# Kernel optimization log

Measured on AMD Instinct MI355X. Metric: run time of the kernel, lower is better.

The kernel has to match this reference:

```python
import jax, jax.numpy as jnp
from jax import lax
import numpy as np

NA, NC = 3, 1
CONF_THRESH, IOU_THRESH = 0.5, 0.5


def _conv(x, w, b, pad):
    y = lax.conv_general_dilated(x, w, (1, 1), [(pad, pad), (pad, pad)],
                                 dimension_numbers=('NCHW', 'OIHW', 'NCHW'))
    return y + b[None, :, None, None]


def _maxpool2(x):
    return lax.reduce_window(x, -jnp.inf, lax.max, (1, 1, 2, 2), (1, 1, 2, 2), 'VALID')


def _stream(x, w1, b1, w2, b2):
    x = _maxpool2(jax.nn.relu(_conv(x, w1, b1, 1)))
    x = _maxpool2(jax.nn.relu(_conv(x, w2, b2, 1)))
    return x


def _pairwise_iou(b):
    # b: [N,4] in (x1,y1,x2,y2); matches torchvision box_iou (no area clamp)
    x1, y1, x2, y2 = b[:, 0], b[:, 1], b[:, 2], b[:, 3]
    area = (x2 - x1) * (y2 - y1)
    ix1 = jnp.maximum(x1[:, None], x1[None, :])
    iy1 = jnp.maximum(y1[:, None], y1[None, :])
    ix2 = jnp.minimum(x2[:, None], x2[None, :])
    iy2 = jnp.minimum(y2[:, None], y2[None, :])
    inter = jnp.clip(ix2 - ix1, 0.0) * jnp.clip(iy2 - iy1, 0.0)
    return inter / (area[:, None] + area[None, :] - inter)


def _nms_keep(boxes, scores, conf_keep, iou_thresh):
    # Greedy NMS over a fixed, small N; returns bool keep mask (conf + NMS).
    n = boxes.shape[0]
    order = jnp.argsort(-jnp.where(conf_keep, scores, -jnp.inf))
    iou = _pairwise_iou(boxes[order])  # [N,N] in score order
    idx = jnp.arange(n)

    def body(i, state):
        keep, suppressed = state
        valid = jnp.logical_not(suppressed[i])
        keep = keep.at[i].set(valid)
        suppressed = suppressed | (valid & (iou[i] > iou_thresh) & (idx > i))
        return keep, suppressed

    keep_sorted, _ = lax.fori_loop(0, n, body,
                                   (jnp.zeros(n, bool), jnp.zeros(n, bool)))
    keep = jnp.zeros(n, bool).at[order].set(keep_sorted)
    return keep & conf_keep


def setup_inputs() -> dict:
    key = jax.random.key(0)
    ks = jax.random.split(key, 14)
    s = 0.05
    inp = {
        'x': jax.random.normal(ks[0], (8, 3, 512, 512), jnp.float32),
        'rgb_w1': jax.random.normal(ks[1], (32, 3, 3, 3), jnp.float32) * s,
        'rgb_b1': jnp.zeros((32,), jnp.float32),
        'rgb_w2': jax.random.normal(ks[2], (64, 32, 3, 3), jnp.float32) * s,
        'rgb_b2': jnp.zeros((64,), jnp.float32),
        'ir_w1': jax.random.normal(ks[3], (32, 3, 3, 3), jnp.float32) * s,
        'ir_b1': jnp.zeros((32,), jnp.float32),
        'ir_w2': jax.random.normal(ks[4], (64, 32, 3, 3), jnp.float32) * s,
        'ir_b2': jnp.zeros((64,), jnp.float32),
        'fuse_w': jax.random.normal(ks[5], (128, 128, 3, 3), jnp.float32) * s,
        'fuse_b': jnp.zeros((128,), jnp.float32),
        'det_w': jax.random.normal(ks[6], (NA * (5 + NC), 128, 1, 1), jnp.float32),
        'det_b': jax.random.normal(ks[7], (NA * (5 + NC),), jnp.float32),
    }
    return inp


def reference(x, rgb_w1, rgb_b1, rgb_w2, rgb_b2,
              ir_w1, ir_b1, ir_w2, ir_b2,
              fuse_w, fuse_b, det_w, det_b):
    f1 = _stream(x, rgb_w1, rgb_b1, rgb_w2, rgb_b2)   # [B,64,H/4,W/4]
    f2 = _stream(x, ir_w1, ir_b1, ir_w2, ir_b2)       # [B,64,H/4,W/4]
    f = jnp.concatenate([f1, f2], axis=1)             # [B,128,H/4,W/4]
    f = jax.nn.relu(_conv(f, fuse_w, fuse_b, 1))
    f = jnp.mean(f, axis=(2, 3), keepdims=True)       # AdaptiveAvgPool2d((1,1))
    p = _conv(f, det_w, det_b, 0)                     # [B,18,1,1]
    B, C, H, W = p.shape
    p = p.reshape(B, NA, 5 + NC, H, W).transpose(0, 1, 3, 4, 2)  # [B,na,H,W,5+nc]
    boxes = p[..., :4].reshape(B, -1, 4)              # [B, na*H*W, 4]
    scores = jax.nn.sigmoid(p[..., 4]).reshape(B, -1) # [B, na*H*W]
    conf_keep = scores > CONF_THRESH
    keep = jax.vmap(_nms_keep, in_axes=(0, 0, 0, None))(boxes, scores, conf_keep,
                                                        IOU_THRESH)
    # Fixed-shape equivalent of the per-image variable-length preds list:
    # preds[b] == boxes[b][keep[b]].
    return p, boxes, scores, keep
```

## Files before the change

kernel.cpp:

```cpp
#include <hip/hip_runtime.h>
#include <math.h>


typedef __bf16 bf16x8 __attribute__((ext_vector_type(8)));
typedef float f32x4 __attribute__((ext_vector_type(4)));

static __device__ __forceinline__ ushort f2bf(float f) {
    unsigned u = __float_as_uint(f);
    unsigned r = (u + 0x7fffu + ((u >> 16) & 1u)) >> 16;
    return (ushort)r;
}
static __device__ __forceinline__ float bf2f(ushort h) {
    return __uint_as_float(((unsigned)h) << 16);
}

__global__ __launch_bounds__(256) void conv1_pool(
    const float* __restrict__ x, const float* __restrict__ w,
    const float* __restrict__ bias, ushort* __restrict__ C1h,
    ushort* __restrict__ C1l)
{
    __shared__ float s[3 * 34 * 34];
    const int b = blockIdx.z;
    const int tileX = blockIdx.x, tileY = blockIdx.y;
    const int tid = threadIdx.x;
    const int tx = tid & 15, ty = tid >> 4;
    const int ih0 = tileY * 32 - 1, iw0 = tileX * 32 - 1;

    for (int i = tid; i < 3 * 34 * 34; i += 256) {
        int c = i / 1156, r = i % 1156;
        int y = r / 34, xx = r % 34;
        int ih = ih0 + y, iw = iw0 + xx;
        float v = 0.f;
        if (ih >= 0 && ih < 512 && iw >= 0 && iw < 512)
            v = x[((b * 3 + c) * 512 + ih) * 512 + iw];
        s[i] = v;
    }
    __syncthreads();

    float in[3][4][4];
#pragma unroll
    for (int c = 0; c < 3; ++c)
#pragma unroll
        for (int dy = 0; dy < 4; ++dy)
#pragma unroll
            for (int dx = 0; dx < 4; ++dx)
                in[c][dy][dx] = s[c * 1156 + (2 * ty + dy) * 34 + (2 * tx + dx)];

    const int oh = tileY * 16 + ty, ow = tileX * 16 + tx;
    __attribute__((aligned(16))) ushort hb[32];
    __attribute__((aligned(16))) ushort lb[32];
#pragma unroll
    for (int oc = 0; oc < 32; ++oc) {
        const float bv = bias[oc];
        float m = -INFINITY;
#pragma unroll
        for (int py = 0; py < 2; ++py)
#pragma unroll
            for (int px = 0; px < 2; ++px) {
                float a = 0.f;
#pragma unroll
                for (int c = 0; c < 3; ++c)
#pragma unroll
                    for (int ky = 0; ky < 3; ++ky)
#pragma unroll
                        for (int kx = 0; kx < 3; ++kx)
                            a = fmaf(w[((oc * 3 + c) * 3 + ky) * 3 + kx],
                                     in[c][py + ky][px + kx], a);
                m = fmaxf(m, a);
            }
        m = fmaxf(m + bv, 0.f);
        ushort h = f2bf(m);
        hb[oc] = h;
        lb[oc] = f2bf(m - bf2f(h));
    }
    size_t base = ((size_t)((b * 256 + oh) * 256 + ow)) << 5;
    uint4* dh = (uint4*)(C1h + base);
    uint4* dl = (uint4*)(C1l + base);
#pragma unroll
    for (int k = 0; k < 4; ++k) {
        dh[k] = *(const uint4*)&hb[k * 8];
        dl[k] = *(const uint4*)&lb[k * 8];
    }
}

__global__ __launch_bounds__(256) void conv2_mfma(
    const ushort* __restrict__ C1h, const ushort* __restrict__ C1l,
    const float* __restrict__ w2, const float* __restrict__ bias,
    ushort* __restrict__ Ahi, ushort* __restrict__ Alo, int stream_base)
{
    __shared__ char lds[40960];
    ushort* Bh = (ushort*)lds;
    ushort* Bl = (ushort*)(lds + 20480);
    float (*pool)[32][64] = (float (*)[32][64])lds;

    const int seg = blockIdx.x, Y = blockIdx.y, b = blockIdx.z;
    const int tid = threadIdx.x, wsub = tid >> 6, lane = tid & 63;
    const int n = lane & 15, q = lane >> 4;
    const int yc = 2 * Y + (wsub & 1);
    const int wx0 = seg * 128 + (wsub >> 1) * 64;

    const uint4 zero4 = make_uint4(0u, 0u, 0u, 0u);

    auto stageB = [&](int t0, int ntap) {
        for (int i = tid; i < ntap * 2048; i += 256) {
            int t = t0 + (i >> 11), r = i & 2047;
            float v = w2[r * 9 + t];
            ushort h = f2bf(v);
            Bh[i] = h;
            Bl[i] = f2bf(v - bf2f(h));
        }
    };

    auto loadA = [&](int t, uint4* aH, uint4* aL) {
        int ky = t / 3, kx = t - ky * 3;
        int yy = yc + ky - 1;
        bool yok = (yy >= 0) & (yy < 256);
#pragma unroll
        for (int mt = 0; mt < 4; ++mt) {
            int xp = wx0 + mt * 16 + n + kx - 1;
            bool ok = yok & (xp >= 0) & (xp < 256);
            int yyc = ok ? yy : 0, xpc = ok ? xp : 0;
            size_t off = (((size_t)((b * 256 + yyc) * 256 + xpc)) << 5) + q * 8;
            aH[mt] = ok ? *(const uint4*)(C1h + off) : zero4;
            aL[mt] = ok ? *(const uint4*)(C1l + off) : zero4;
        }
    };

    f32x4 acc[4][4];
#pragma unroll
    for (int mt = 0; mt < 4; ++mt)
#pragma unroll
        for (int nt = 0; nt < 4; ++nt) acc[mt][nt] = (f32x4){0.f, 0.f, 0.f, 0.f};

    uint4 aH[4], aL[4];
    loadA(0, aH, aL);
    stageB(0, 5);
    __syncthreads();

    for (int t = 0; t < 9; ++t) {
        if (t == 5) {
            __syncthreads();
            stageB(5, 4);
            __syncthreads();
        }
        const int rel = (t < 5) ? t : t - 5;
        uint4 cH[4], cL[4];
#pragma unroll
        for (int mt = 0; mt < 4; ++mt) { cH[mt] = aH[mt]; cL[mt] = aL[mt]; }
        if (t + 1 < 9) loadA(t + 1, aH, aL);
        bf16x8 bh[4], bl[4];
#pragma unroll
        for (int nt = 0; nt < 4; ++nt) {
            int off = rel * 2048 + (nt * 16 + n) * 32 + q * 8;
            bh[nt] = __builtin_bit_cast(bf16x8, *(const uint4*)&Bh[off]);
            bl[nt] = __builtin_bit_cast(bf16x8, *(const uint4*)&Bl[off]);
        }
#pragma unroll
        for (int mt = 0; mt < 4; ++mt) {
            bf16x8 ah = __builtin_bit_cast(bf16x8, cH[mt]);
#pragma unroll
            for (int nt = 0; nt < 4; ++nt)
                acc[mt][nt] = __builtin_amdgcn_mfma_f32_16x16x32_bf16(ah, bh[nt], acc[mt][nt], 0, 0, 0);
        }
#pragma unroll
        for (int mt = 0; mt < 4; ++mt) {
            bf16x8 ah = __builtin_bit_cast(bf16x8, cH[mt]);
#pragma unroll
            for (int nt = 0; nt < 4; ++nt)
                acc[mt][nt] = __builtin_amdgcn_mfma_f32_16x16x32_bf16(ah, bl[nt], acc[mt][nt], 0, 0, 0);
        }
#pragma unroll
        for (int mt = 0; mt < 4; ++mt) {
            bf16x8 al = __builtin_bit_cast(bf16x8, cL[mt]);
#pragma unroll
            for (int nt = 0; nt < 4; ++nt)
                acc[mt][nt] = __builtin_amdgcn_mfma_f32_16x16x32_bf16(al, bh[nt], acc[mt][nt], 0, 0, 0);
        }
    }

    __syncthreads();

#pragma unroll
    for (int mt = 0; mt < 4; ++mt)
#pragma unroll
        for (int nt = 0; nt < 4; ++nt) {
            int oc = nt * 16 + n;
            int plx = mt * 8 + q * 2;
            pool[wsub][plx][oc]     = fmaxf(acc[mt][nt][0], acc[mt][nt][1]);
            pool[wsub][plx + 1][oc] = fmaxf(acc[mt][nt][2], acc[mt][nt][3]);
        }
    __syncthreads();

    {
        int plx = tid >> 2, ocq = tid & 3;
        int wp = plx >> 5, pl = plx & 31;
        __attribute__((aligned(16))) ushort hb[16], lb[16];
#pragma unroll
        for (int e = 0; e < 16; ++e) {
            int oc = ocq * 16 + e;
            float v = fmaxf(pool[wp * 2][pl][oc], pool[wp * 2 + 1][pl][oc]);
            v = fmaxf(v + bias[oc], 0.f);
            ushort h = f2bf(v);
            hb[e] = h;
            lb[e] = f2bf(v - bf2f(h));
        }
        int gx = seg * 64 + plx;
        int cpl = (stream_base >> 5) + (ocq >> 1);
        int cho = (ocq & 1) * 16;
        size_t base = (((size_t)(((b * 4 + cpl) * 128 + Y) * 128 + gx)) << 5) + cho;
        uint4* dh = (uint4*)(Ahi + base);
        uint4* dl = (uint4*)(Alo + base);
        dh[0] = *(const uint4*)&hb[0];
        dh[1] = *(const uint4*)&hb[8];
        dl[0] = *(const uint4*)&lb[0];
        dl[1] = *(const uint4*)&lb[8];
    }
}

__global__ __launch_bounds__(256) void wprep(
    const float* __restrict__ fw, ushort* __restrict__ Whi,
    ushort* __restrict__ Wlo)
{
    int idx = blockIdx.x * 256 + threadIdx.x;
    if (idx >= 147456) return;
    int kk = idx & 31;
    int oc = (idx >> 5) & 127;
    int ct = idx >> 12;
    int c = ct / 9, t = ct - c * 9;
    int ic = c * 32 + kk;
    int ky = t / 3, kx = t - ky * 3;
    float v = fw[((oc * 128 + ic) * 3 + ky) * 3 + kx];
    ushort h = f2bf(v);
    Whi[idx] = h;
    Wlo[idx] = f2bf(v - bf2f(h));
}

__global__ __launch_bounds__(256, 2) void fuse_mfma(
    const ushort* __restrict__ Ahi, const ushort* __restrict__ Alo,
    const ushort* __restrict__ Whi, const ushort* __restrict__ Wlo,
    const float* __restrict__ bias, float* __restrict__ featsum)
{
    __shared__ float partial[4][128];
    const int b = blockIdx.x, ypair = blockIdx.y;
    const int tid = threadIdx.x, wsub = tid >> 6, lane = tid & 63;
    const int n = lane & 15, q = lane >> 4;
    const int y = ypair * 2 + (wsub >> 1);
    const int xbase = (wsub & 1) * 64;

    f32x4 acc[4][8];
#pragma unroll
    for (int mt = 0; mt < 4; ++mt)
#pragma unroll
        for (int g = 0; g < 8; ++g) acc[mt][g] = (f32x4){0.f, 0.f, 0.f, 0.f};

    const uint4 zero4 = make_uint4(0u, 0u, 0u, 0u);

    auto loadA = [&](int tc, uint4* oh, uint4* ol) {
        int c = tc / 9, t = tc - c * 9;
        int ky = t / 3, kx = t - ky * 3;
        int yy = y + ky - 1;
        bool yok = (yy >= 0) & (yy < 128);
#pragma unroll
        for (int mt = 0; mt < 4; ++mt) {
            int xp = xbase + mt * 16 + n + kx - 1;
            bool ok = yok & (xp >= 0) & (xp < 128);
            int yyc = ok ? yy : 0, xpc = ok ? xp : 0;
            size_t aoff = (((size_t)(((b * 4 + c) * 128 + yyc) * 128 + xpc)) << 5) + q * 8;
            oh[mt] = ok ? *(const uint4*)(Ahi + aoff) : zero4;
            ol[mt] = ok ? *(const uint4*)(Alo + aoff) : zero4;
        }
    };

    uint4 pAh[4], pAl[4];
    loadA(0, pAh, pAl);

    const ushort* WhiB = Whi + n * 32 + q * 8;
    const ushort* WloB = Wlo + n * 32 + q * 8;

    uint4 nBh[4], nBl[4];
#pragma unroll
    for (int j = 0; j < 4; ++j) {
        nBh[j] = *(const uint4*)(WhiB + j * 512);
        nBl[j] = *(const uint4*)(WloB + j * 512);
    }

    for (int tc = 0; tc < 36; ++tc) {
        uint4 cAh[4], cAl[4];
#pragma unroll
        for (int mt = 0; mt < 4; ++mt) { cAh[mt] = pAh[mt]; cAl[mt] = pAl[mt]; }
        if (tc + 1 < 36) loadA(tc + 1, pAh, pAl);
#pragma unroll
        for (int g = 0; g < 8; ++g) {
            const int slot = g & 3;
            bf16x8 bh = __builtin_bit_cast(bf16x8, nBh[slot]);
            bf16x8 bl = __builtin_bit_cast(bf16x8, nBl[slot]);
            {
                size_t off = (size_t)(tc * 8 + g + 4) * 512;
                nBh[slot] = *(const uint4*)(WhiB + off);
                nBl[slot] = *(const uint4*)(WloB + off);
            }
#pragma unroll
            for (int mt = 0; mt < 4; ++mt) {
                bf16x8 ah = __builtin_bit_cast(bf16x8, cAh[mt]);
                acc[mt][g] = __builtin_amdgcn_mfma_f32_16x16x32_bf16(ah, bh, acc[mt][g], 0, 0, 0);
            }
#pragma unroll
            for (int mt = 0; mt < 4; ++mt) {
                bf16x8 ah = __builtin_bit_cast(bf16x8, cAh[mt]);
                acc[mt][g] = __builtin_amdgcn_mfma_f32_16x16x32_bf16(ah, bl, acc[mt][g], 0, 0, 0);
            }
#pragma unroll
            for (int mt = 0; mt < 4; ++mt) {
                bf16x8 al = __builtin_bit_cast(bf16x8, cAl[mt]);
                acc[mt][g] = __builtin_amdgcn_mfma_f32_16x16x32_bf16(al, bh, acc[mt][g], 0, 0, 0);
            }
        }
    }

#pragma unroll
    for (int g = 0; g < 8; ++g) {
        float bv = bias[g * 16 + n];
        float v = 0.f;
#pragma unroll
        for (int mt = 0; mt < 4; ++mt)
#pragma unroll
            for (int r = 0; r < 4; ++r) v += fmaxf(acc[mt][g][r] + bv, 0.f);
        v += __shfl_xor(v, 16);
        v += __shfl_xor(v, 32);
        if (lane < 16) partial[wsub][g * 16 + lane] = v;
    }
    __syncthreads();
    if (tid < 128) {
        float v = partial[0][tid] + partial[1][tid] + partial[2][tid] + partial[3][tid];
        atomicAdd(&featsum[b * 128 + tid], v);
    }
}

__global__ void det_nms(const float* __restrict__ featsum,
                        const float* __restrict__ dw, const float* __restrict__ db,
                        float* __restrict__ out)
{
    const int b = threadIdx.x;
    if (b >= 8) return;
    const float inv = 1.0f / 16384.0f;

    float p[18];
    for (int j = 0; j < 18; ++j) {
        float a = db[j];
        const float* wp = &dw[j * 128];
        const float* f = &featsum[b * 128];
        for (int c = 0; c < 128; ++c) a = fmaf(wp[c], f[c] * inv, a);
        p[j] = a;
    }
    for (int a = 0; a < 3; ++a)
        for (int e = 0; e < 6; ++e) out[b * 18 + a * 6 + e] = p[a * 6 + e];

    float bx[3][4], sc[3];
    bool ck[3];
    for (int a = 0; a < 3; ++a) {
        for (int k = 0; k < 4; ++k) {
            bx[a][k] = p[a * 6 + k];
            out[144 + b * 12 + a * 4 + k] = bx[a][k];
        }
        float sg = 1.f / (1.f + expf(-p[a * 6 + 4]));
        sc[a] = sg;
        ck[a] = sg > 0.5f;
        out[240 + b * 3 + a] = sg;
    }

    float key[3];
    int order[3];
    bool used[3] = {false, false, false};
    for (int a = 0; a < 3; ++a) key[a] = ck[a] ? sc[a] : -INFINITY;
    for (int i = 0; i < 3; ++i) {
        int best = -1;
        float bk = 0.f;
        for (int a = 0; a < 3; ++a) {
            if (used[a]) continue;
            if (best < 0 || key[a] > bk) { best = a; bk = key[a]; }
        }
        order[i] = best;
        used[best] = true;
    }

    float X1[3], Y1[3], X2[3], Y2[3], AR[3];
    for (int i = 0; i < 3; ++i) {
        int o = order[i];
        X1[i] = bx[o][0]; Y1[i] = bx[o][1];
        X2[i] = bx[o][2]; Y2[i] = bx[o][3];
        AR[i] = (X2[i] - X1[i]) * (Y2[i] - Y1[i]);
    }
    bool suppressed[3] = {false, false, false}, keep_s[3];
    for (int i = 0; i < 3; ++i) {
        bool valid = !suppressed[i];
        keep_s[i] = valid;
        if (valid) {
            for (int j = i + 1; j < 3; ++j) {
                float ix1 = fmaxf(X1[i], X1[j]), iy1 = fmaxf(Y1[i], Y1[j]);
                float ix2 = fminf(X2[i], X2[j]), iy2 = fminf(Y2[i], Y2[j]);
                float inter = fmaxf(ix2 - ix1, 0.f) * fmaxf(iy2 - iy1, 0.f);
                float iou = inter / (AR[i] + AR[j] - inter);
                if (iou > 0.5f) suppressed[j] = true;
            }
        }
    }
    bool keep[3];
    for (int i = 0; i < 3; ++i) keep[order[i]] = keep_s[i];
    for (int a = 0; a < 3; ++a)
        out[264 + b * 3 + a] = (keep[a] && ck[a]) ? 1.f : 0.f;
}

__global__ void zero_feat(float* __restrict__ p)
{
    int i = blockIdx.x * 256 + threadIdx.x;
    if (i < 1024) p[i] = 0.f;
}

extern "C" void kernel_launch(void* const* d_in, const int* in_sizes, int n_in,
                              void* d_out, int out_size, void* d_ws, size_t ws_size,
                              hipStream_t stream)
{
    const float* x      = (const float*)d_in[0];
    const float* rgb_w1 = (const float*)d_in[1];
    const float* rgb_b1 = (const float*)d_in[2];
    const float* rgb_w2 = (const float*)d_in[3];
    const float* rgb_b2 = (const float*)d_in[4];
    const float* ir_w1  = (const float*)d_in[5];
    const float* ir_b1  = (const float*)d_in[6];
    const float* ir_w2  = (const float*)d_in[7];
    const float* ir_b2  = (const float*)d_in[8];
    const float* fuse_w = (const float*)d_in[9];
    const float* fuse_b = (const float*)d_in[10];
    const float* det_w  = (const float*)d_in[11];
    const float* det_b  = (const float*)d_in[12];
    float* out = (float*)d_out;

    char* ws = (char*)d_ws;
    ushort* C1h  = (ushort*)(ws);
    ushort* C1l  = (ushort*)(ws + 33554432);
    ushort* Whi  = (ushort*)(ws);
    ushort* Wlo  = (ushort*)(ws + 299008);
    float*  feat = (float*)(ws + 598016);
    ushort* Ahi  = (ushort*)(ws + 67108864);
    ushort* Alo  = (ushort*)(ws + 100663296);

    dim3 blk(256);
    hipLaunchKernelGGL(conv1_pool, dim3(16, 16, 8), blk, 0, stream, x, rgb_w1, rgb_b1, C1h, C1l);
    hipLaunchKernelGGL(conv2_mfma, dim3(2, 128, 8), blk, 0, stream, C1h, C1l, rgb_w2, rgb_b2, Ahi, Alo, 0);
    hipLaunchKernelGGL(conv1_pool, dim3(16, 16, 8), blk, 0, stream, x, ir_w1, ir_b1, C1h, C1l);
    hipLaunchKernelGGL(conv2_mfma, dim3(2, 128, 8), blk, 0, stream, C1h, C1l, ir_w2, ir_b2, Ahi, Alo, 64);
    hipLaunchKernelGGL(wprep, dim3(576), blk, 0, stream, fuse_w, Whi, Wlo);
    hipLaunchKernelGGL(zero_feat, dim3(4), blk, 0, stream, feat);
    hipLaunchKernelGGL(fuse_mfma, dim3(8, 64), blk, 0, stream, Ahi, Alo, Whi, Wlo, fuse_b, feat);
    hipLaunchKernelGGL(det_nms, dim3(1), dim3(64), 0, stream, feat, det_w, det_b, out);
}
```

Before: 571.0 us.

## Rewrite first conv+pool as bf16x3 MFMA implicit GEMM

Replaces the scalar FMA conv1+maxpool kernel with an MFMA implicit-GEMM version. Input pixels and weights are split into hi/lo bf16 pairs, and three MFMA products emulate fp32 accuracy. The 2x2 pool runs through LDS before the bf16 hi/lo output is written. A small weight prep kernel packs the 27-tap weights, padded to 32. K padding wastes some MFMA work, and a block now covers only one output row, which raises the number of input halo reloads.

```diff
diff --git a/kernel.cpp b/kernel.cpp
--- a/kernel.cpp
+++ b/kernel.cpp
@@ -14,72 +14,138 @@
     return __uint_as_float(((unsigned)h) << 16);
 }
 
-__global__ __launch_bounds__(256) void conv1_pool(
-    const float* __restrict__ x, const float* __restrict__ w,
+__global__ __launch_bounds__(256) void w1prep(
+    const float* __restrict__ w_rgb, const float* __restrict__ w_ir,
+    uint* __restrict__ W1p)
+{
+    int i = blockIdx.x * 256 + threadIdx.x;
+    if (i >= 2048) return;
+    int s = i >> 10, r = i & 1023;
+    int oc = r >> 5, k = r & 31;
+    const float* w = s ? w_ir : w_rgb;
+    float v = (k < 27) ? w[oc * 27 + k] : 0.f;
+    ushort h = f2bf(v);
+    W1p[i] = (uint)h | ((uint)f2bf(v - bf2f(h)) << 16);
+}
+
+__global__ __launch_bounds__(256) void conv1_mfma(
+    const float* __restrict__ x, const uint* __restrict__ W1p,
     const float* __restrict__ bias, ushort* __restrict__ C1h,
     ushort* __restrict__ C1l)
 {
-    __shared__ float s[3 * 34 * 34];
-    const int b = blockIdx.z;
-    const int tileX = blockIdx.x, tileY = blockIdx.y;
-    const int tid = threadIdx.x;
-    const int tx = tid & 15, ty = tid >> 4;
-    const int ih0 = tileY * 32 - 1, iw0 = tileX * 32 - 1;
-
-    for (int i = tid; i < 3 * 34 * 34; i += 256) {
-        int c = i / 1156, r = i % 1156;
-        int y = r / 34, xx = r % 34;
-        int ih = ih0 + y, iw = iw0 + xx;
+    __shared__ uint S[3 * 4 * 132];
+    __shared__ float pool[4][32][32];
+
+    const int seg = blockIdx.x, Y = blockIdx.y, b = blockIdx.z;
+    const int tid = threadIdx.x, wsub = tid >> 6, lane = tid & 63;
+    const int n = lane & 15, q = lane >> 4;
+
+    uint4 bu0a = *(const uint4*)&W1p[n * 32 + q * 8];
+    uint4 bu0b = *(const uint4*)&W1p[n * 32 + q * 8 + 4];
+    uint4 bu1a = *(const uint4*)&W1p[(16 + n) * 32 + q * 8];
+    uint4 bu1b = *(const uint4*)&W1p[(16 + n) * 32 + q * 8 + 4];
+
+    const int ih0 = 2 * Y - 1, iw0 = seg * 128 - 1;
+    for (int i = tid; i < 1584; i += 256) {
+        int c = i / 528, rem = i - c * 528;
+        int r = rem / 132, cc = rem - r * 132;
+        int ih = ih0 + r, iw = iw0 + cc;
         float v = 0.f;
-        if (ih >= 0 && ih < 512 && iw >= 0 && iw < 512)
+        if (cc < 130 && ih >= 0 && ih < 512 && iw >= 0 && iw < 512)
             v = x[((b * 3 + c) * 512 + ih) * 512 + iw];
-        s[i] = v;
+        ushort h = f2bf(v);
+        S[i] = (uint)h | ((uint)f2bf(v - bf2f(h)) << 16);
+    }
+
+    uint4 bh0v, bl0v, bh1v, bl1v;
+    {
+        uint u0[8], u1[8];
+        *(uint4*)&u0[0] = bu0a; *(uint4*)&u0[4] = bu0b;
+        *(uint4*)&u1[0] = bu1a; *(uint4*)&u1[4] = bu1b;
+        uint* bh0 = (uint*)&bh0v; uint* bl0 = (uint*)&bl0v;
+        uint* bh1 = (uint*)&bh1v; uint* bl1 = (uint*)&bl1v;
+#pragma unroll
+        for (int j = 0; j < 4; ++j) {
+            bh0[j] = (u0[2 * j] & 0xffffu) | (u0[2 * j + 1] << 16);
+            bl0[j] = (u0[2 * j] >> 16) | (u0[2 * j + 1] & 0xffff0000u);
+            bh1[j] = (u1[2 * j] & 0xffffu) | (u1[2 * j + 1] << 16);
+            bl1[j] = (u1[2 * j] >> 16) | (u1[2 * j + 1] & 0xffff0000u);
+        }
+    }
+    bf16x8 Bh0 = __builtin_bit_cast(bf16x8, bh0v);
+    bf16x8 Bl0 = __builtin_bit_cast(bf16x8, bl0v);
+    bf16x8 Bh1 = __builtin_bit_cast(bf16x8, bh1v);
+    bf16x8 Bl1 = __builtin_bit_cast(bf16x8, bl1v);
+
+    int idx[8];
+    const int off0 = (wsub & 1) * 132 + (wsub >> 1) * 64 + n;
+#pragma unroll
+    for (int e = 0; e < 8; ++e) {
+        int k = q * 8 + e;
+        int c = (k >= 18) ? ((k >= 27) ? 3 : 2) : ((k >= 9) ? 1 : 0);
+        int t = k - c * 9;
+        int ky = (t >= 6) ? 2 : ((t >= 3) ? 1 : 0);
+        int kx = t - ky * 3;
+        idx[e] = (k < 27) ? ((c * 4 + ky) * 132 + kx + off0) : 0;
     }
     __syncthreads();
 
-    float in[3][4][4];
-#pragma unroll
-    for (int c = 0; c < 3; ++c)
-#pragma unroll
-        for (int dy = 0; dy < 4; ++dy)
-#pragma unroll
-            for (int dx = 0; dx < 4; ++dx)
-                in[c][dy][dx] = s[c * 1156 + (2 * ty + dy) * 34 + (2 * tx + dx)];
-
-    const int oh = tileY * 16 + ty, ow = tileX * 16 + tx;
-    __attribute__((aligned(16))) ushort hb[32];
-    __attribute__((aligned(16))) ushort lb[32];
-#pragma unroll
-    for (int oc = 0; oc < 32; ++oc) {
-        const float bv = bias[oc];
-        float m = -INFINITY;
-#pragma unroll
-        for (int py = 0; py < 2; ++py)
-#pragma unroll
-            for (int px = 0; px < 2; ++px) {
-                float a = 0.f;
-#pragma unroll
-                for (int c = 0; c < 3; ++c)
-#pragma unroll
-                    for (int ky = 0; ky < 3; ++ky)
-#pragma unroll
-                        for (int kx = 0; kx < 3; ++kx)
-                            a = fmaf(w[((oc * 3 + c) * 3 + ky) * 3 + kx],
-                                     in[c][py + ky][px + kx], a);
-                m = fmaxf(m, a);
-            }
-        m = fmaxf(m + bv, 0.f);
-        ushort h = f2bf(m);
-        hb[oc] = h;
-        lb[oc] = f2bf(m - bf2f(h));
-    }
-    size_t base = ((size_t)((b * 256 + oh) * 256 + ow)) << 5;
-    uint4* dh = (uint4*)(C1h + base);
-    uint4* dl = (uint4*)(C1l + base);
-#pragma unroll
-    for (int k = 0; k < 4; ++k) {
-        dh[k] = *(const uint4*)&hb[k * 8];
-        dl[k] = *(const uint4*)&lb[k * 8];
+    f32x4 acc[4][2];
+#pragma unroll
+    for (int mt = 0; mt < 4; ++mt)
+#pragma unroll
+        for (int nt = 0; nt < 2; ++nt) acc[mt][nt] = (f32x4){0.f, 0.f, 0.f, 0.f};
+
+#pragma unroll
+    for (int mt = 0; mt < 4; ++mt) {
+        uint u[8];
+#pragma unroll
+        for (int e = 0; e < 8; ++e) u[e] = S[idx[e] + mt * 16];
+        uint4 ahv, alv;
+        uint* ah = (uint*)&ahv;
+        uint* al = (uint*)&alv;
+#pragma unroll
+        for (int j = 0; j < 4; ++j) {
+            ah[j] = (u[2 * j] & 0xffffu) | (u[2 * j + 1] << 16);
+            al[j] = (u[2 * j] >> 16) | (u[2 * j + 1] & 0xffff0000u);
+        }
+        bf16x8 Ah = __builtin_bit_cast(bf16x8, ahv);
+        bf16x8 Al = __builtin_bit_cast(bf16x8, alv);
+        acc[mt][0] = __builtin_amdgcn_mfma_f32_16x16x32_bf16(Ah, Bh0, acc[mt][0], 0, 0, 0);
+        acc[mt][1] = __builtin_amdgcn_mfma_f32_16x16x32_bf16(Ah, Bh1, acc[mt][1], 0, 0, 0);
+        acc[mt][0] = __builtin_amdgcn_mfma_f32_16x16x32_bf16(Ah, Bl0, acc[mt][0], 0, 0, 0);
+        acc[mt][1] = __builtin_amdgcn_mfma_f32_16x16x32_bf16(Ah, Bl1, acc[mt][1], 0, 0, 0);
+        acc[mt][0] = __builtin_amdgcn_mfma_f32_16x16x32_bf16(Al, Bh0, acc[mt][0], 0, 0, 0);
+        acc[mt][1] = __builtin_amdgcn_mfma_f32_16x16x32_bf16(Al, Bh1, acc[mt][1], 0, 0, 0);
+    }
+
+#pragma unroll
+    for (int mt = 0; mt < 4; ++mt)
+#pragma unroll
+        for (int nt = 0; nt < 2; ++nt) {
+            int oc = nt * 16 + n;
+            int plx = mt * 8 + q * 2;
+            pool[wsub][plx][oc]     = fmaxf(acc[mt][nt][0], acc[mt][nt][1]);
+            pool[wsub][plx + 1][oc] = fmaxf(acc[mt][nt][2], acc[mt][nt][3]);
+        }
+    __syncthreads();
+    {
+        int plx = tid >> 2, ocq = tid & 3;
+        int wp = plx >> 5, pl = plx & 31;
+        __attribute__((aligned(16))) ushort hb[8], lb[8];
+#pragma unroll
+        for (int e = 0; e < 8; ++e) {
+            int oc = ocq * 8 + e;
+            float v = fmaxf(pool[wp * 2][pl][oc], pool[wp * 2 + 1][pl][oc]);
+            v = fmaxf(v + bias[oc], 0.f);
+            ushort h = f2bf(v);
+            hb[e] = h;
+            lb[e] = f2bf(v - bf2f(h));
+        }
+        int ow = seg * 64 + plx;
+        size_t base = (((size_t)((b * 256 + Y) * 256 + ow)) << 5) + ocq * 8;
+        *(uint4*)(C1h + base) = *(const uint4*)hb;
+        *(uint4*)(C1l + base) = *(const uint4*)lb;
     }
 }
 
@@ -443,11 +509,13 @@
     float*  feat = (float*)(ws + 598016);
     ushort* Ahi  = (ushort*)(ws + 67108864);
     ushort* Alo  = (ushort*)(ws + 100663296);
+    uint*   W1p  = (uint*)(ws + 134209536);
 
     dim3 blk(256);
-    hipLaunchKernelGGL(conv1_pool, dim3(16, 16, 8), blk, 0, stream, x, rgb_w1, rgb_b1, C1h, C1l);
+    hipLaunchKernelGGL(w1prep, dim3(8), blk, 0, stream, rgb_w1, ir_w1, W1p);
+    hipLaunchKernelGGL(conv1_mfma, dim3(4, 256, 8), blk, 0, stream, x, W1p, rgb_b1, C1h, C1l);
     hipLaunchKernelGGL(conv2_mfma, dim3(2, 128, 8), blk, 0, stream, C1h, C1l, rgb_w2, rgb_b2, Ahi, Alo, 0);
-    hipLaunchKernelGGL(conv1_pool, dim3(16, 16, 8), blk, 0, stream, x, ir_w1, ir_b1, C1h, C1l);
+    hipLaunchKernelGGL(conv1_mfma, dim3(4, 256, 8), blk, 0, stream, x, W1p + 1024, ir_b1, C1h, C1l);
     hipLaunchKernelGGL(conv2_mfma, dim3(2, 128, 8), blk, 0, stream, C1h, C1l, ir_w2, ir_b2, Ahi, Alo, 64);
     hipLaunchKernelGGL(wprep, dim3(576), blk, 0, stream, fuse_w, Whi, Wlo);
     hipLaunchKernelGGL(zero_feat, dim3(4), blk, 0, stream, feat);
```

New measurement: 512.6 us. 1.11x faster.
